# Kernel optimization log

Measured on AMD Instinct MI355X. Metric: run time of the kernel, lower is better.

The kernel has to match this reference:

```python
import jax, jax.numpy as jnp
import numpy as np

B, T, C, H = 2, 4096, 1024, 16
D = C // H
SEGMENTS = ((512, 1), (1024, 2), (2048, 4))  # (segment_length w, dilation r) per LongNet config


def setup_inputs() -> dict:
    key = jax.random.key(0)
    ks = jax.random.split(key, 12)
    s = 0.02
    return {
        "x": jax.random.normal(ks[0], (B, T, C), jnp.float32),
        # outer fused qkv projection (c_attn), stored as [in, out] so y = x @ W + b
        "c_attn_w": jax.random.normal(ks[1], (C, 3 * C), jnp.float32) * s,
        "c_attn_b": jnp.zeros((3 * C,), jnp.float32),
        # inner torchscale MultiheadAttention projections
        "q_w": jax.random.normal(ks[2], (C, C), jnp.float32) * s,
        "q_b": jnp.zeros((C,), jnp.float32),
        "k_w": jax.random.normal(ks[3], (C, C), jnp.float32) * s,
        "k_b": jnp.zeros((C,), jnp.float32),
        "v_w": jax.random.normal(ks[4], (C, C), jnp.float32) * s,
        "v_b": jnp.zeros((C,), jnp.float32),
        "o_w": jax.random.normal(ks[5], (C, C), jnp.float32) * s,
        "o_b": jnp.zeros((C,), jnp.float32),
    }


def _branch(q, k, v, w, r):
    """One dilated-attention branch: segment length w, dilation r.
    q,k,v: [B,H,T,D] (q pre-scaled). Heads use offset = head % r (LongNet).
    Returns (out_full [B,H,T,D], lse_full [B,H,T]) scattered back to full positions.
    """
    b, h_, t, d = q.shape
    n_seg, eff = t // w, w // r
    h = jnp.arange(h_)
    idx = (h % r)[:, None] + jnp.arange(eff)[None, :] * r            # [H, eff] within-segment indices
    pos = jnp.arange(n_seg)[None, :, None] * w + idx[:, None, :]     # [H, n_seg, eff] absolute positions
    hh = h[:, None, None]
    qg = q[:, hh, pos]                                               # [B,H,n_seg,eff,D]
    kg = k[:, hh, pos]
    vg = v[:, hh, pos]
    scores = jnp.einsum('bhsid,bhsjd->bhsij', qg, kg)
    causal = jnp.tril(jnp.ones((eff, eff), bool))                    # order preserved under strided subsampling
    scores = jnp.where(causal, scores, jnp.finfo(scores.dtype).min)
    m = scores.max(-1, keepdims=True)
    p = jnp.exp(scores - m)
    s = p.sum(-1, keepdims=True)
    o = jnp.einsum('bhsij,bhsjd->bhsid', p, vg) / s
    lse = m[..., 0] + jnp.log(s[..., 0])                             # [B,H,n_seg,eff]
    out_full = jnp.zeros((b, h_, t, d), q.dtype).at[:, hh, pos].set(o)
    lse_full = jnp.full((b, h_, t), -1e30, q.dtype).at[:, hh, pos].set(lse)
    return out_full, lse_full


def _forward(x, c_attn_w, c_attn_b, q_w, q_b, k_w, k_b, v_w, v_b, o_w, o_b):
    b, t, c = x.shape
    qkv = x @ c_attn_w + c_attn_b
    qx, kx, vx = jnp.split(qkv, 3, axis=-1)
    q = (qx @ q_w + q_b).reshape(b, t, H, D).transpose(0, 2, 1, 3) * (D ** -0.5)
    k = (kx @ k_w + k_b).reshape(b, t, H, D).transpose(0, 2, 1, 3)
    v = (vx @ v_w + v_b).reshape(b, t, H, D).transpose(0, 2, 1, 3)
    outs, lses = zip(*[_branch(q, k, v, w, r) for w, r in SEGMENTS])
    O = jnp.stack(outs)                                              # [S,B,H,T,D]
    L = jnp.stack(lses)                                              # [S,B,H,T]
    # LongNet combination: weight each branch by its softmax denominator (via lse)
    m = L.max(0)
    wts = jnp.exp(L - m)                                             # [S,B,H,T]
    y = (wts[..., None] * O).sum(0) / wts.sum(0)[..., None]          # [B,H,T,D]
    y = y.transpose(0, 2, 1, 3).reshape(b, t, c)
    return y @ o_w + o_b


def reference(x, c_attn_w, c_attn_b, q_w, q_b, k_w, k_b, v_w, v_b, o_w, o_b):
    return _forward(x, c_attn_w, c_attn_b, q_w, q_b, k_w, k_b, v_w, v_b, o_w, o_b)
```

## Files before the change

### kernel.cpp

```cpp
#include <hip/hip_runtime.h>
#include <hip/hip_bf16.h>

typedef __bf16 bf16x8 __attribute__((ext_vector_type(8)));
typedef float  f32x4  __attribute__((ext_vector_type(4)));

__device__ __forceinline__ unsigned short f2bf(float f) {
    union { float f; unsigned int u; } v; v.f = f;
    return (unsigned short)((v.u + 0x8000u) >> 16);
}
__device__ __forceinline__ float bf2f(unsigned short h) {
    union { unsigned int u; float f; } v; v.u = ((unsigned int)h) << 16;
    return v.f;
}

typedef __attribute__((address_space(3))) unsigned int lds_u32_t;
typedef const __attribute__((address_space(1))) unsigned int glb_u32_t;
__device__ __forceinline__ void gl_lds16(const void* g, void* l) {
    __builtin_amdgcn_global_load_lds((glb_u32_t*)g, (lds_u32_t*)l, 16, 0, 0);
}

__global__ void k_cast(const float* __restrict__ in, unsigned short* __restrict__ out, int n) {
    int i = (blockIdx.x * blockDim.x + threadIdx.x) * 4;
    if (i + 3 < n) {
        float4 v = *reinterpret_cast<const float4*>(in + i);
        ushort4 o;
        o.x = f2bf(v.x); o.y = f2bf(v.y); o.z = f2bf(v.z); o.w = f2bf(v.w);
        *reinterpret_cast<ushort4*>(out + i) = o;
    }
}

__global__ void k_transpose4(const float* __restrict__ s0, const float* __restrict__ s1,
                             const float* __restrict__ s2, const float* __restrict__ s3,
                             unsigned short* __restrict__ d0, unsigned short* __restrict__ d1,
                             unsigned short* __restrict__ d2, unsigned short* __restrict__ d3) {
    __shared__ float tile[32][33];
    int z = blockIdx.z;
    const float* in = (z == 0) ? s0 : (z == 1) ? s1 : (z == 2) ? s2 : s3;
    unsigned short* out = (z == 0) ? d0 : (z == 1) ? d1 : (z == 2) ? d2 : d3;
    int n0 = blockIdx.x * 32, k0 = blockIdx.y * 32;
    int tx = threadIdx.x, ty = threadIdx.y;
    #pragma unroll
    for (int i = 0; i < 4; ++i)
        tile[ty + i * 8][tx] = in[(size_t)(k0 + ty + i * 8) * 1024 + n0 + tx];
    __syncthreads();
    #pragma unroll
    for (int i = 0; i < 4; ++i)
        out[(size_t)(n0 + ty + i * 8) * 1024 + k0 + tx] = f2bf(tile[tx][ty + i * 8]);
}

__global__ __launch_bounds__(256) void k_gemm(
    const unsigned short* __restrict__ A, int lda,
    const unsigned short* __restrict__ Bt, int ldb,
    const float* __restrict__ bias,
    void* __restrict__ out,
    int M, int N, int K, int mode, float scale)
{
    __shared__ unsigned short As[128 * 32];
    __shared__ unsigned short Bs[128 * 32];
    int tid  = threadIdx.x;
    int lane = tid & 63, wv = tid >> 6;
    int quad = lane >> 4, l16 = lane & 15;

    int nwg = gridDim.x * gridDim.y;
    int lin = blockIdx.y * gridDim.x + blockIdx.x;
    int bx = blockIdx.x, by = blockIdx.y;
    if ((nwg & 7) == 0) {
        int swz = (lin & 7) * (nwg >> 3) + (lin >> 3);
        bx = swz % gridDim.x;
        by = swz / gridDim.x;
    }
    int bm = by * 128, bn = bx * 128;
    int wm = (wv >> 1) * 64,  wn = (wv & 1) * 64;

    f32x4 acc[4][4] = {};
    int srow = tid >> 2, scol = (tid & 3) * 8;

    for (int k0 = 0; k0 < K; k0 += 32) {
        #pragma unroll
        for (int s = 0; s < 2; ++s) {
            int row = s * 64 + srow;
            gl_lds16(&A[(size_t)(bm + row) * lda + k0 + scol], &As[(s * 256 + wv * 64) * 8]);
            gl_lds16(&Bt[(size_t)(bn + row) * ldb + k0 + scol], &Bs[(s * 256 + wv * 64) * 8]);
        }
        __syncthreads();
        bf16x8 af[4], bfv[4];
        #pragma unroll
        for (int mi = 0; mi < 4; ++mi)
            af[mi] = *reinterpret_cast<const bf16x8*>(&As[(wm + mi * 16 + l16) * 32 + quad * 8]);
        #pragma unroll
        for (int ni = 0; ni < 4; ++ni)
            bfv[ni] = *reinterpret_cast<const bf16x8*>(&Bs[(wn + ni * 16 + l16) * 32 + quad * 8]);
        #pragma unroll
        for (int mi = 0; mi < 4; ++mi)
            #pragma unroll
            for (int ni = 0; ni < 4; ++ni)
                acc[mi][ni] = __builtin_amdgcn_mfma_f32_16x16x32_bf16(bfv[ni], af[mi], acc[mi][ni], 0, 0, 0);
        __syncthreads();
    }

    #pragma unroll
    for (int mi = 0; mi < 4; ++mi) {
        int row = bm + wm + mi * 16 + l16;
        #pragma unroll
        for (int ni = 0; ni < 4; ++ni) {
            int col0 = bn + wn + ni * 16 + quad * 4;
            float4 b4 = *reinterpret_cast<const float4*>(&bias[col0]);
            float v0 = (acc[mi][ni][0] + b4.x) * scale;
            float v1 = (acc[mi][ni][1] + b4.y) * scale;
            float v2 = (acc[mi][ni][2] + b4.z) * scale;
            float v3 = (acc[mi][ni][3] + b4.w) * scale;
            if (mode == 0) {
                ushort4 o4; o4.x = f2bf(v0); o4.y = f2bf(v1); o4.z = f2bf(v2); o4.w = f2bf(v3);
                *reinterpret_cast<ushort4*>(&reinterpret_cast<unsigned short*>(out)[(size_t)row * N + col0]) = o4;
            } else {
                float4 o4; o4.x = v0; o4.y = v1; o4.z = v2; o4.w = v3;
                *reinterpret_cast<float4*>(&reinterpret_cast<float*>(out)[(size_t)row * N + col0]) = o4;
            }
        }
    }
}

__global__ __launch_bounds__(256) void k_foldw(
    const unsigned short* __restrict__ wT3,
    const unsigned short* __restrict__ WcB,
    unsigned short* __restrict__ Weff)
{
    __shared__ unsigned short As[128 * 32];
    __shared__ unsigned short Bs[128 * 32];
    int z = blockIdx.z;
    const unsigned short* A  = wT3 + (size_t)z * 1024 * 1024;
    const unsigned short* Bt = WcB + z * 1024;
    unsigned short* out = Weff + (size_t)z * 1024 * 1024;
    float scale = (z == 0) ? 0.1803368801f : 1.f;

    int tid  = threadIdx.x;
    int lane = tid & 63, wv = tid >> 6;
    int quad = lane >> 4, l16 = lane & 15;
    int bm = blockIdx.y * 128, bn = blockIdx.x * 128;
    int wm = (wv >> 1) * 64,  wn = (wv & 1) * 64;

    f32x4 acc[4][4] = {};
    int srow = tid >> 2, scol = (tid & 3) * 8;

    for (int k0 = 0; k0 < 1024; k0 += 32) {
        #pragma unroll
        for (int s = 0; s < 2; ++s) {
            int row = s * 64 + srow;
            gl_lds16(&A[(size_t)(bm + row) * 1024 + k0 + scol], &As[(s * 256 + wv * 64) * 8]);
            gl_lds16(&Bt[(size_t)(bn + row) * 3072 + k0 + scol], &Bs[(s * 256 + wv * 64) * 8]);
        }
        __syncthreads();
        bf16x8 af[4], bfv[4];
        #pragma unroll
        for (int mi = 0; mi < 4; ++mi)
            af[mi] = *reinterpret_cast<const bf16x8*>(&As[(wm + mi * 16 + l16) * 32 + quad * 8]);
        #pragma unroll
        for (int ni = 0; ni < 4; ++ni)
            bfv[ni] = *reinterpret_cast<const bf16x8*>(&Bs[(wn + ni * 16 + l16) * 32 + quad * 8]);
        #pragma unroll
        for (int mi = 0; mi < 4; ++mi)
            #pragma unroll
            for (int ni = 0; ni < 4; ++ni)
                acc[mi][ni] = __builtin_amdgcn_mfma_f32_16x16x32_bf16(bfv[ni], af[mi], acc[mi][ni], 0, 0, 0);
        __syncthreads();
    }

    #pragma unroll
    for (int mi = 0; mi < 4; ++mi) {
        int row = bm + wm + mi * 16 + l16;
        #pragma unroll
        for (int ni = 0; ni < 4; ++ni) {
            int col0 = bn + wn + ni * 16 + quad * 4;
            ushort4 o4;
            o4.x = f2bf(acc[mi][ni][0] * scale);
            o4.y = f2bf(acc[mi][ni][1] * scale);
            o4.z = f2bf(acc[mi][ni][2] * scale);
            o4.w = f2bf(acc[mi][ni][3] * scale);
            *reinterpret_cast<ushort4*>(&out[(size_t)row * 1024 + col0]) = o4;
        }
    }
}

__global__ void k_foldb(const unsigned short* __restrict__ wT3, const float* __restrict__ bc,
                        const float* __restrict__ qb, const float* __restrict__ kb,
                        const float* __restrict__ vb, float* __restrict__ beff)
{
    int id = blockIdx.x * blockDim.x + threadIdx.x;
    int z = id >> 10, n = id & 1023;
    const unsigned short* row = wT3 + (size_t)z * 1024 * 1024 + (size_t)n * 1024;
    const float* b2 = (z == 0) ? qb : (z == 1) ? kb : vb;
    float s = 0.f;
    for (int c = 0; c < 1024; ++c) s += bc[z * 1024 + c] * bf2f(row[c]);
    s += b2[n];
    if (z == 0) s *= 0.1803368801f;
    beff[id] = s;
}

__global__ __launch_bounds__(256) void k_gemm3(
    const unsigned short* __restrict__ A,
    const unsigned short* __restrict__ Weff,
    const float* __restrict__ beff,
    unsigned short* __restrict__ Qg, unsigned short* __restrict__ Kg,
    unsigned short* __restrict__ Vtg)
{
    __shared__ unsigned short As[128 * 32];
    __shared__ unsigned short Bs[128 * 32];

    int tid  = threadIdx.x;
    int lane = tid & 63, wv = tid >> 6;
    int quad = lane >> 4, l16 = lane & 15;

    int nwg = gridDim.x * gridDim.y * gridDim.z;
    int lin = (blockIdx.z * gridDim.y + blockIdx.y) * gridDim.x + blockIdx.x;
    int swz = (lin & 7) * (nwg >> 3) + (lin >> 3);
    int bx  = swz % gridDim.x;
    int tmp = swz / gridDim.x;
    int by  = tmp % gridDim.y;
    int z   = tmp / gridDim.y;

    const unsigned short* Bt = Weff + (size_t)z * 1024 * 1024;
    const float* bias = beff + z * 1024;

    int bm = by * 128, bn = bx * 128;
    int wm = (wv >> 1) * 64,  wn = (wv & 1) * 64;

    f32x4 acc[4][4] = {};
    int srow = tid >> 2, scol = (tid & 3) * 8;

    for (int k0 = 0; k0 < 1024; k0 += 32) {
        #pragma unroll
        for (int s = 0; s < 2; ++s) {
            int row = s * 64 + srow;
            gl_lds16(&A[(size_t)(bm + row) * 1024 + k0 + scol], &As[(s * 256 + wv * 64) * 8]);
            gl_lds16(&Bt[(size_t)(bn + row) * 1024 + k0 + scol], &Bs[(s * 256 + wv * 64) * 8]);
        }
        __syncthreads();
        bf16x8 af[4], bfv[4];
        #pragma unroll
        for (int mi = 0; mi < 4; ++mi)
            af[mi] = *reinterpret_cast<const bf16x8*>(&As[(wm + mi * 16 + l16) * 32 + quad * 8]);
        #pragma unroll
        for (int ni = 0; ni < 4; ++ni)
            bfv[ni] = *reinterpret_cast<const bf16x8*>(&Bs[(wn + ni * 16 + l16) * 32 + quad * 8]);
        if (z < 2) {
            #pragma unroll
            for (int mi = 0; mi < 4; ++mi)
                #pragma unroll
                for (int ni = 0; ni < 4; ++ni)
                    acc[mi][ni] = __builtin_amdgcn_mfma_f32_16x16x32_bf16(bfv[ni], af[mi], acc[mi][ni], 0, 0, 0);
        } else {
            #pragma unroll
            for (int mi = 0; mi < 4; ++mi)
                #pragma unroll
                for (int ni = 0; ni < 4; ++ni)
                    acc[mi][ni] = __builtin_amdgcn_mfma_f32_16x16x32_bf16(af[mi], bfv[ni], acc[mi][ni], 0, 0, 0);
        }
        __syncthreads();
    }

    if (z < 2) {
        unsigned short* dst = (z == 0) ? Qg : Kg;
        int hh = (bn + wn) >> 6;
        #pragma unroll
        for (int mi = 0; mi < 4; ++mi) {
            int trow = bm + wm + mi * 16 + l16;
            int b = trow >> 12, t = trow & 4095;
            int bh = b * 16 + hh;
            int slot0 = t >> 9,         idx0 = t & 511;
            int slot1 = 8 + (t >> 10),  idx1 = (t & 1023) >> 1;
            int slot2 = 12 + (t >> 11), idx2 = (t & 2047) >> 2;
            bool c1 = ((t ^ hh) & 1) == 0;
            bool c2 = ((t ^ hh) & 3) == 0;
            size_t r0 = ((size_t)(slot0 * 32 + bh) * 512 + idx0) * 64;
            size_t r1 = ((size_t)(slot1 * 32 + bh) * 512 + idx1) * 64;
            size_t r2 = ((size_t)(slot2 * 32 + bh) * 512 + idx2) * 64;
            #pragma unroll
            for (int ni = 0; ni < 4; ++ni) {
                int d0 = ni * 16 + quad * 4;
                float4 b4 = *reinterpret_cast<const float4*>(&bias[bn + wn + d0]);
                ushort4 o4;
                o4.x = f2bf(acc[mi][ni][0] + b4.x);
                o4.y = f2bf(acc[mi][ni][1] + b4.y);
                o4.z = f2bf(acc[mi][ni][2] + b4.z);
                o4.w = f2bf(acc[mi][ni][3] + b4.w);
                *reinterpret_cast<ushort4*>(&dst[r0 + d0]) = o4;
                if (c1) *reinterpret_cast<ushort4*>(&dst[r1 + d0]) = o4;
                if (c2) *reinterpret_cast<ushort4*>(&dst[r2 + d0]) = o4;
            }
        }
    } else {
        int h_glob = (bn + wn) >> 6;
        int j1 = h_glob & 1;
        int j2 = h_glob & 3;
        #pragma unroll
        for (int ni = 0; ni < 4; ++ni) {
            int d = ni * 16 + l16;
            float bsv = bias[bn + wn + d];
            #pragma unroll
            for (int mi = 0; mi < 4; ++mi) {
                int t0g = bm + wm + mi * 16 + quad * 4;
                int b = t0g >> 12, t0 = t0g & 4095;
                int bh = b * 16 + h_glob;
                unsigned short val[4];
                #pragma unroll
                for (int ri = 0; ri < 4; ++ri) val[ri] = f2bf(acc[mi][ni][ri] + bsv);
                {
                    int slot = t0 >> 9;
                    size_t base = ((size_t)(slot * 32 + bh) * 64 + d) * 512 + (t0 & 511);
                    *reinterpret_cast<ushort4*>(&Vtg[base]) = *reinterpret_cast<const ushort4*>(val);
                }
                {
                    int slot = 8 + (t0 >> 10);
                    int idx = ((t0 + j1) & 1023) >> 1;
                    size_t base = ((size_t)(slot * 32 + bh) * 64 + d) * 512 + idx;
                    ushort2 o2; o2.x = val[j1]; o2.y = val[j1 + 2];
                    *reinterpret_cast<ushort2*>(&Vtg[base]) = o2;
                }
                {
                    int slot = 12 + (t0 >> 11);
                    int idx = ((t0 + j2) & 2047) >> 2;
                    Vtg[((size_t)(slot * 32 + bh) * 64 + d) * 512 + idx] = val[j2];
                }
            }
        }
    }
}

__global__ __launch_bounds__(256, 3) void k_attn(
    const unsigned short* __restrict__ Qg,
    const unsigned short* __restrict__ Kg,
    const unsigned short* __restrict__ Vtg,
    unsigned short* __restrict__ Og,
    float* __restrict__ Lg)
{
    __shared__ unsigned short Ks[2][64 * 72];
    __shared__ unsigned short Vs[2][64 * 72];

    int tid  = threadIdx.x;
    int lane = tid & 63, wv = tid >> 6;
    int quad = lane >> 4, l16 = lane & 15;
    int q8   = quad << 3;
    int pq = blockIdx.x, ys = blockIdx.y, bh = blockIdx.z;
    int jt_end = 2 * (3 - pq) + 1;
    size_t sb = (size_t)(ys * 32 + bh) * (512 * 64);
    const unsigned short* qp = Qg + sb;
    const unsigned short* kp = Kg + sb;
    const unsigned short* vp = Vtg + sb;
    unsigned short* op = Og + sb;
    float* lp = Lg + (size_t)(ys * 32 + bh) * 512;

    int rw[2] = { pq * 128 + wv * 32, (3 - pq) * 128 + wv * 32 };

    int srow = tid >> 3, sc8 = (tid & 7) * 8;
    int prow = ((srow >> 2) & 1) * 16 + ((srow >> 3) & 3) * 4 + (srow & 3);
    uint4 kr[2], vr[2];
    {
        #pragma unroll
        for (int s = 0; s < 2; ++s) {
            int row = s * 32 + srow;
            kr[s] = *reinterpret_cast<const uint4*>(&kp[(size_t)row * 64 + sc8]);
            vr[s] = *reinterpret_cast<const uint4*>(&vp[(size_t)row * 512 + sc8]);
        }
    }

    bf16x8 qf[2][2][2];
    #pragma unroll
    for (int qi = 0; qi < 2; ++qi)
        #pragma unroll
        for (int m16 = 0; m16 < 2; ++m16)
            #pragma unroll
            for (int kk = 0; kk < 2; ++kk)
                qf[qi][m16][kk] = *reinterpret_cast<const bf16x8*>(
                    &qp[(size_t)(rw[qi] + m16 * 16 + l16) * 64 + kk * 32 + quad * 8]);

    f32x4 acc[2][2][4] = {};
    float l4[2][2] = {};

    for (int jt = 0; jt <= jt_end; ++jt) {
        unsigned short* Kb = &Ks[jt & 1][0];
        unsigned short* Vb = &Vs[jt & 1][0];
        #pragma unroll
        for (int s = 0; s < 2; ++s) {
            *reinterpret_cast<uint4*>(&Kb[(s * 32 + prow) * 72 + sc8]) = kr[s];
            *reinterpret_cast<uint4*>(&Vb[(s * 32 + srow) * 72 + sc8]) = vr[s];
        }
        if (jt < jt_end) {
            #pragma unroll
            for (int s = 0; s < 2; ++s) {
                int row = s * 32 + srow;
                kr[s] = *reinterpret_cast<const uint4*>(&kp[(size_t)((jt + 1) * 64 + row) * 64 + sc8]);
                vr[s] = *reinterpret_cast<const uint4*>(&vp[(size_t)row * 512 + (jt + 1) * 64 + sc8]);
            }
        }
        __syncthreads();

        #pragma unroll
        for (int qi = 0; qi < 2; ++qi) {
            #pragma unroll
            for (int m16 = 0; m16 < 2; ++m16) {
                int rowbase = rw[qi] + m16 * 16;
                if (jt * 64 > rowbase + 15) continue;

                f32x4 sacc[4];
                __builtin_amdgcn_s_setprio(1);
                #pragma unroll
                for (int nt = 0; nt < 4; ++nt) {
                    bf16x8 b0 = *reinterpret_cast<const bf16x8*>(&Kb[(nt * 16 + l16) * 72 + quad * 8]);
                    bf16x8 b1 = *reinterpret_cast<const bf16x8*>(&Kb[(nt * 16 + l16) * 72 + 32 + quad * 8]);
                    f32x4 s4 = {};
                    s4 = __builtin_amdgcn_mfma_f32_16x16x32_bf16(b0, qf[qi][m16][0], s4, 0, 0, 0);
                    s4 = __builtin_amdgcn_mfma_f32_16x16x32_bf16(b1, qf[qi][m16][1], s4, 0, 0, 0);
                    sacc[nt] = s4;
                }
                __builtin_amdgcn_s_setprio(0);

                if (jt * 64 + 63 > rowbase) {
                    int qrow = rowbase + l16;
                    #pragma unroll
                    for (int nt = 0; nt < 4; ++nt)
                        #pragma unroll
                        for (int ri = 0; ri < 4; ++ri) {
                            int kj = jt * 64 + (nt >> 1) * 32 + (nt & 1) * 4 + q8 + ri;
                            if (kj > qrow) sacc[nt][ri] = -1e30f;
                        }
                }
                float ls = 0.f;
                #pragma unroll
                for (int nt = 0; nt < 4; ++nt)
                    #pragma unroll
                    for (int ri = 0; ri < 4; ++ri) {
                        float p = __builtin_amdgcn_exp2f(sacc[nt][ri]);
                        sacc[nt][ri] = p;
                        ls += p;
                    }
                l4[qi][m16] += ls;

                union { unsigned int u[4]; bf16x8 v; } p0u, p1u;
                asm("v_cvt_pk_bf16_f32 %0, %1, %2" : "=v"(p0u.u[0]) : "v"(sacc[0][0]), "v"(sacc[0][1]));
                asm("v_cvt_pk_bf16_f32 %0, %1, %2" : "=v"(p0u.u[1]) : "v"(sacc[0][2]), "v"(sacc[0][3]));
                asm("v_cvt_pk_bf16_f32 %0, %1, %2" : "=v"(p0u.u[2]) : "v"(sacc[1][0]), "v"(sacc[1][1]));
                asm("v_cvt_pk_bf16_f32 %0, %1, %2" : "=v"(p0u.u[3]) : "v"(sacc[1][2]), "v"(sacc[1][3]));
                asm("v_cvt_pk_bf16_f32 %0, %1, %2" : "=v"(p1u.u[0]) : "v"(sacc[2][0]), "v"(sacc[2][1]));
                asm("v_cvt_pk_bf16_f32 %0, %1, %2" : "=v"(p1u.u[1]) : "v"(sacc[2][2]), "v"(sacc[2][3]));
                asm("v_cvt_pk_bf16_f32 %0, %1, %2" : "=v"(p1u.u[2]) : "v"(sacc[3][0]), "v"(sacc[3][1]));
                asm("v_cvt_pk_bf16_f32 %0, %1, %2" : "=v"(p1u.u[3]) : "v"(sacc[3][2]), "v"(sacc[3][3]));

                __builtin_amdgcn_s_setprio(1);
                #pragma unroll
                for (int dt = 0; dt < 4; ++dt) {
                    bf16x8 v0 = *reinterpret_cast<const bf16x8*>(&Vb[(dt * 16 + l16) * 72 + quad * 8]);
                    bf16x8 v1 = *reinterpret_cast<const bf16x8*>(&Vb[(dt * 16 + l16) * 72 + 32 + quad * 8]);
                    f32x4 a4 = acc[qi][m16][dt];
                    a4 = __builtin_amdgcn_mfma_f32_16x16x32_bf16(p0u.v, v0, a4, 0, 0, 0);
                    a4 = __builtin_amdgcn_mfma_f32_16x16x32_bf16(p1u.v, v1, a4, 0, 0, 0);
                    acc[qi][m16][dt] = a4;
                }
                __builtin_amdgcn_s_setprio(0);
            }
        }
    }

    #pragma unroll
    for (int qi = 0; qi < 2; ++qi)
        #pragma unroll
        for (int m16 = 0; m16 < 2; ++m16) {
            int rowb = rw[qi] + m16 * 16;
            float L = l4[qi][m16];
            L += __shfl_xor(L, 16);
            L += __shfl_xor(L, 32);
            float inv[4];
            #pragma unroll
            for (int ri = 0; ri < 4; ++ri)
                inv[ri] = 1.f / __shfl(L, quad * 4 + ri);
            #pragma unroll
            for (int dt = 0; dt < 4; ++dt)
                #pragma unroll
                for (int ri = 0; ri < 4; ++ri) {
                    int row = rowb + quad * 4 + ri;
                    op[(size_t)row * 64 + dt * 16 + l16] = f2bf(acc[qi][m16][dt][ri] * inv[ri]);
                }
            if (lane < 16)
                lp[rowb + l16] = __logf(L);
        }
}

__global__ void k_combine(const unsigned short* __restrict__ Og,
                          const float* __restrict__ Lg,
                          unsigned short* __restrict__ yb)
{
    int g   = blockIdx.x * blockDim.x + threadIdx.x;
    int row = g >> 3;
    int d0  = (g & 7) * 8;
    int bh = row >> 12, t = row & 4095;
    int b = bh >> 4, h = bh & 15;

    int slot0 = t >> 9,         idx0 = t & 511;
    int slot1 = 8 + (t >> 10),  idx1 = (t & 1023) >> 1;
    int slot2 = 12 + (t >> 11), idx2 = (t & 2047) >> 2;
    size_t r0 = (size_t)(slot0 * 32 + bh) * 512 + idx0;
    size_t r1 = (size_t)(slot1 * 32 + bh) * 512 + idx1;
    size_t r2 = (size_t)(slot2 * 32 + bh) * 512 + idx2;
    bool c1 = ((t ^ h) & 1) == 0;
    bool c2 = ((t ^ h) & 3) == 0;

    float L0 = Lg[r0];
    float L1 = c1 ? Lg[r1] : -1e30f;
    float L2 = c2 ? Lg[r2] : -1e30f;
    float m  = fmaxf(L0, fmaxf(L1, L2));
    float w0 = __expf(L0 - m), w1 = __expf(L1 - m), w2 = __expf(L2 - m);
    float inv = 1.f / (w0 + w1 + w2);

    uint4 v0 = *reinterpret_cast<const uint4*>(&Og[r0 * 64 + d0]);
    uint4 v1 = *reinterpret_cast<const uint4*>(&Og[r1 * 64 + d0]);
    uint4 v2 = *reinterpret_cast<const uint4*>(&Og[r2 * 64 + d0]);
    const unsigned short* p0 = reinterpret_cast<const unsigned short*>(&v0);
    const unsigned short* p1 = reinterpret_cast<const unsigned short*>(&v1);
    const unsigned short* p2 = reinterpret_cast<const unsigned short*>(&v2);
    unsigned short o[8];
    #pragma unroll
    for (int u = 0; u < 8; ++u)
        o[u] = f2bf((w0 * bf2f(p0[u]) + w1 * bf2f(p1[u]) + w2 * bf2f(p2[u])) * inv);
    size_t yidx = (((size_t)b * 4096 + t) * 1024) + (size_t)h * 64 + d0;
    *reinterpret_cast<uint4*>(&yb[yidx]) = *reinterpret_cast<const uint4*>(o);
}

extern "C" void kernel_launch(void* const* d_in, const int* in_sizes, int n_in,
                              void* d_out, int out_size, void* d_ws, size_t ws_size,
                              hipStream_t stream)
{
    const float* x        = (const float*)d_in[0];
    const float* c_attn_w = (const float*)d_in[1];
    const float* c_attn_b = (const float*)d_in[2];
    const float* q_w      = (const float*)d_in[3];
    const float* q_b      = (const float*)d_in[4];
    const float* k_w      = (const float*)d_in[5];
    const float* k_b      = (const float*)d_in[6];
    const float* v_w      = (const float*)d_in[7];
    const float* v_b      = (const float*)d_in[8];
    const float* o_w      = (const float*)d_in[9];
    const float* o_b      = (const float*)d_in[10];

    char* ws = (char*)d_ws;
    size_t off = 0;
    auto alloc = [&](size_t bytes) -> char* {
        char* p = ws + off; off += (bytes + 255) & ~(size_t)255; return p;
    };
    const size_t GSZ = 14ull * 32 * 512 * 64;
    unsigned short* xb    = (unsigned short*)alloc(8192ull * 1024 * 2);
    unsigned short* WcB   = (unsigned short*)alloc(1024ull * 3072 * 2);
    unsigned short* wqT   = (unsigned short*)alloc(1024ull * 1024 * 2);
    unsigned short* wkT   = (unsigned short*)alloc(1024ull * 1024 * 2);
    unsigned short* wvT   = (unsigned short*)alloc(1024ull * 1024 * 2);
    unsigned short* woT   = (unsigned short*)alloc(1024ull * 1024 * 2);
    unsigned short* Weff  = (unsigned short*)alloc(3ull * 1024 * 1024 * 2);
    float*          beff  = (float*)alloc(3ull * 1024 * 4);
    unsigned short* Qg    = (unsigned short*)alloc(GSZ * 2);
    unsigned short* Kg    = (unsigned short*)alloc(GSZ * 2);
    unsigned short* Vtg   = (unsigned short*)alloc(GSZ * 2);
    unsigned short* Og    = (unsigned short*)alloc(GSZ * 2);
    float*          Lg    = (float*)alloc(14ull * 32 * 512 * 4);
    unsigned short* yb    = xb;
    (void)wkT; (void)wvT;

    k_cast<<<(8192 * 1024) / 1024, 256, 0, stream>>>(x, xb, 8192 * 1024);
    k_cast<<<(1024 * 3072) / 1024, 256, 0, stream>>>(c_attn_w, WcB, 1024 * 3072);
    k_transpose4<<<dim3(32, 32, 4), dim3(32, 8), 0, stream>>>(q_w, k_w, v_w, o_w, wqT, wkT, wvT, woT);
    k_foldw<<<dim3(8, 8, 3), 256, 0, stream>>>(wqT, WcB, Weff);
    k_foldb<<<12, 256, 0, stream>>>(wqT, c_attn_b, q_b, k_b, v_b, beff);
    k_gemm3<<<dim3(8, 64, 3), 256, 0, stream>>>(xb, Weff, beff, Qg, Kg, Vtg);
    k_attn<<<dim3(2, 14, 32), 256, 0, stream>>>(Qg, Kg, Vtg, Og, Lg);
    k_combine<<<4096, 256, 0, stream>>>(Og, Lg, yb);
    k_gemm<<<dim3(8, 64), 256, 0, stream>>>(yb, 1024, woT, 1024, o_b, d_out, 8192, 1024, 1024, 2, 1.f);
}
```

Baseline: 382.0 us.

## Stage QKV epilogue through LDS for coalesced scatter; parallelize bias fold per wave

The QKV GEMM epilogue now writes the bf16 tile into padded shared memory and then emits 16-byte coalesced stores for each dilated-segment layout (Q/K rows and transposed V), replacing scattered 8/4/2-byte strided global writes. Separately, the bias-folding kernel goes from one thread per output with a serial 1024-long loop to one wave per output with vectorized loads and a shuffle reduction, launched across 768 blocks. The cost is a larger LDS footprint, an extra barrier, and strided LDS gathers for the dilated V layouts.

```diff
diff --git a/kernel.cpp b/kernel.cpp
--- a/kernel.cpp
+++ b/kernel.cpp
@@ -181,19 +181,35 @@
     }
 }
 
-__global__ void k_foldb(const unsigned short* __restrict__ wT3, const float* __restrict__ bc,
-                        const float* __restrict__ qb, const float* __restrict__ kb,
-                        const float* __restrict__ vb, float* __restrict__ beff)
+__global__ __launch_bounds__(256) void k_foldb(
+    const unsigned short* __restrict__ wT3, const float* __restrict__ bc,
+    const float* __restrict__ qb, const float* __restrict__ kb,
+    const float* __restrict__ vb, float* __restrict__ beff)
 {
-    int id = blockIdx.x * blockDim.x + threadIdx.x;
+    int wv = threadIdx.x >> 6, lane = threadIdx.x & 63;
+    int id = blockIdx.x * 4 + wv;
     int z = id >> 10, n = id & 1023;
     const unsigned short* row = wT3 + (size_t)z * 1024 * 1024 + (size_t)n * 1024;
-    const float* b2 = (z == 0) ? qb : (z == 1) ? kb : vb;
+    const float* bcz = bc + z * 1024;
     float s = 0.f;
-    for (int c = 0; c < 1024; ++c) s += bc[z * 1024 + c] * bf2f(row[c]);
-    s += b2[n];
-    if (z == 0) s *= 0.1803368801f;
-    beff[id] = s;
+    #pragma unroll
+    for (int it = 0; it < 2; ++it) {
+        int c0 = it * 512 + lane * 8;
+        uint4 v = *reinterpret_cast<const uint4*>(&row[c0]);
+        const unsigned short* pv = reinterpret_cast<const unsigned short*>(&v);
+        float4 f0 = *reinterpret_cast<const float4*>(&bcz[c0]);
+        float4 f1 = *reinterpret_cast<const float4*>(&bcz[c0 + 4]);
+        s += f0.x * bf2f(pv[0]) + f0.y * bf2f(pv[1]) + f0.z * bf2f(pv[2]) + f0.w * bf2f(pv[3]);
+        s += f1.x * bf2f(pv[4]) + f1.y * bf2f(pv[5]) + f1.z * bf2f(pv[6]) + f1.w * bf2f(pv[7]);
+    }
+    s += __shfl_xor(s, 1); s += __shfl_xor(s, 2); s += __shfl_xor(s, 4);
+    s += __shfl_xor(s, 8); s += __shfl_xor(s, 16); s += __shfl_xor(s, 32);
+    if (lane == 0) {
+        const float* b2 = (z == 0) ? qb : (z == 1) ? kb : vb;
+        float r = s + b2[n];
+        if (z == 0) r *= 0.1803368801f;
+        beff[id] = r;
+    }
 }
 
 __global__ __launch_bounds__(256) void k_gemm3(
@@ -203,8 +219,10 @@
     unsigned short* __restrict__ Qg, unsigned short* __restrict__ Kg,
     unsigned short* __restrict__ Vtg)
 {
-    __shared__ unsigned short As[128 * 32];
-    __shared__ unsigned short Bs[128 * 32];
+    __shared__ unsigned short smem[16896];
+    unsigned short* As = smem;
+    unsigned short* Bs = smem + 4096;
+    const int TS = 132;
 
     int tid  = threadIdx.x;
     int lane = tid & 63, wv = tid >> 6;
@@ -213,10 +231,10 @@
     int nwg = gridDim.x * gridDim.y * gridDim.z;
     int lin = (blockIdx.z * gridDim.y + blockIdx.y) * gridDim.x + blockIdx.x;
     int swz = (lin & 7) * (nwg >> 3) + (lin >> 3);
-    int bx  = swz % gridDim.x;
-    int tmp = swz / gridDim.x;
-    int by  = tmp % gridDim.y;
-    int z   = tmp / gridDim.y;
+    int bx  = swz & 7;
+    int tmp = swz >> 3;
+    int by  = tmp & 63;
+    int z   = tmp >> 6;
 
     const unsigned short* Bt = Weff + (size_t)z * 1024 * 1024;
     const float* bias = beff + z * 1024;
@@ -258,70 +276,121 @@
         __syncthreads();
     }
 
+    unsigned short* T = smem;
+    int b  = bm >> 12, t0 = bm & 4095;
+    int h0 = bn >> 6;
+    int slot0 = t0 >> 9;
+    int slot1 = 8 + (t0 >> 10);
+    int slot2 = 12 + (t0 >> 11);
+
     if (z < 2) {
         unsigned short* dst = (z == 0) ? Qg : Kg;
-        int hh = (bn + wn) >> 6;
         #pragma unroll
         for (int mi = 0; mi < 4; ++mi) {
-            int trow = bm + wm + mi * 16 + l16;
-            int b = trow >> 12, t = trow & 4095;
-            int bh = b * 16 + hh;
-            int slot0 = t >> 9,         idx0 = t & 511;
-            int slot1 = 8 + (t >> 10),  idx1 = (t & 1023) >> 1;
-            int slot2 = 12 + (t >> 11), idx2 = (t & 2047) >> 2;
-            bool c1 = ((t ^ hh) & 1) == 0;
-            bool c2 = ((t ^ hh) & 3) == 0;
-            size_t r0 = ((size_t)(slot0 * 32 + bh) * 512 + idx0) * 64;
-            size_t r1 = ((size_t)(slot1 * 32 + bh) * 512 + idx1) * 64;
-            size_t r2 = ((size_t)(slot2 * 32 + bh) * 512 + idx2) * 64;
+            int tl = wm + mi * 16 + l16;
             #pragma unroll
             for (int ni = 0; ni < 4; ++ni) {
-                int d0 = ni * 16 + quad * 4;
-                float4 b4 = *reinterpret_cast<const float4*>(&bias[bn + wn + d0]);
+                int dl0 = wn + ni * 16 + quad * 4;
+                float4 b4 = *reinterpret_cast<const float4*>(&bias[bn + dl0]);
                 ushort4 o4;
                 o4.x = f2bf(acc[mi][ni][0] + b4.x);
                 o4.y = f2bf(acc[mi][ni][1] + b4.y);
                 o4.z = f2bf(acc[mi][ni][2] + b4.z);
                 o4.w = f2bf(acc[mi][ni][3] + b4.w);
-                *reinterpret_cast<ushort4*>(&dst[r0 + d0]) = o4;
-                if (c1) *reinterpret_cast<ushort4*>(&dst[r1 + d0]) = o4;
-                if (c2) *reinterpret_cast<ushort4*>(&dst[r2 + d0]) = o4;
+                *reinterpret_cast<ushort4*>(&T[tl * TS + dl0]) = o4;
             }
         }
+        __syncthreads();
+        #pragma unroll
+        for (int rep = 0; rep < 8; ++rep) {
+            int c = rep * 256 + tid;
+            int h = c >> 10, rr = c & 1023;
+            int tl = rr >> 3, dseg = (rr & 7) * 8;
+            int bh = b * 16 + h0 + h;
+            size_t base = ((size_t)(slot0 * 32 + bh) * 512 + (t0 & 511) + tl) * 64;
+            *reinterpret_cast<uint4*>(&dst[base + dseg]) =
+                *reinterpret_cast<const uint4*>(&T[tl * TS + h * 64 + dseg]);
+        }
+        #pragma unroll
+        for (int rep = 0; rep < 4; ++rep) {
+            int c = rep * 256 + tid;
+            int h = c >> 9, rr = c & 511;
+            int i = rr >> 3, dseg = (rr & 7) * 8;
+            int hh = h0 + h;
+            int bh = b * 16 + hh;
+            int tl = 2 * i + (hh & 1);
+            size_t base = ((size_t)(slot1 * 32 + bh) * 512 + ((t0 & 1023) >> 1) + i) * 64;
+            *reinterpret_cast<uint4*>(&dst[base + dseg]) =
+                *reinterpret_cast<const uint4*>(&T[tl * TS + h * 64 + dseg]);
+        }
+        #pragma unroll
+        for (int rep = 0; rep < 2; ++rep) {
+            int c = rep * 256 + tid;
+            int h = c >> 8, rr = c & 255;
+            int i = rr >> 3, dseg = (rr & 7) * 8;
+            int hh = h0 + h;
+            int bh = b * 16 + hh;
+            int tl = 4 * i + (hh & 3);
+            size_t base = ((size_t)(slot2 * 32 + bh) * 512 + ((t0 & 2047) >> 2) + i) * 64;
+            *reinterpret_cast<uint4*>(&dst[base + dseg]) =
+                *reinterpret_cast<const uint4*>(&T[tl * TS + h * 64 + dseg]);
+        }
     } else {
-        int h_glob = (bn + wn) >> 6;
-        int j1 = h_glob & 1;
-        int j2 = h_glob & 3;
         #pragma unroll
         for (int ni = 0; ni < 4; ++ni) {
-            int d = ni * 16 + l16;
-            float bsv = bias[bn + wn + d];
+            int dl = wn + ni * 16 + l16;
+            float bsv = bias[bn + dl];
             #pragma unroll
             for (int mi = 0; mi < 4; ++mi) {
-                int t0g = bm + wm + mi * 16 + quad * 4;
-                int b = t0g >> 12, t0 = t0g & 4095;
-                int bh = b * 16 + h_glob;
-                unsigned short val[4];
-                #pragma unroll
-                for (int ri = 0; ri < 4; ++ri) val[ri] = f2bf(acc[mi][ni][ri] + bsv);
-                {
-                    int slot = t0 >> 9;
-                    size_t base = ((size_t)(slot * 32 + bh) * 64 + d) * 512 + (t0 & 511);
-                    *reinterpret_cast<ushort4*>(&Vtg[base]) = *reinterpret_cast<const ushort4*>(val);
-                }
-                {
-                    int slot = 8 + (t0 >> 10);
-                    int idx = ((t0 + j1) & 1023) >> 1;
-                    size_t base = ((size_t)(slot * 32 + bh) * 64 + d) * 512 + idx;
-                    ushort2 o2; o2.x = val[j1]; o2.y = val[j1 + 2];
-                    *reinterpret_cast<ushort2*>(&Vtg[base]) = o2;
-                }
-                {
-                    int slot = 12 + (t0 >> 11);
-                    int idx = ((t0 + j2) & 2047) >> 2;
-                    Vtg[((size_t)(slot * 32 + bh) * 64 + d) * 512 + idx] = val[j2];
-                }
+                int tl0 = wm + mi * 16 + quad * 4;
+                ushort4 o4;
+                o4.x = f2bf(acc[mi][ni][0] + bsv);
+                o4.y = f2bf(acc[mi][ni][1] + bsv);
+                o4.z = f2bf(acc[mi][ni][2] + bsv);
+                o4.w = f2bf(acc[mi][ni][3] + bsv);
+                *reinterpret_cast<ushort4*>(&T[dl * TS + tl0]) = o4;
             }
+        }
+        __syncthreads();
+        #pragma unroll
+        for (int rep = 0; rep < 8; ++rep) {
+            int c = rep * 256 + tid;
+            int h = c >> 10, rr = c & 1023;
+            int d = rr >> 4, seg = (rr & 15) * 8;
+            int bh = b * 16 + h0 + h;
+            size_t base = ((size_t)(slot0 * 32 + bh) * 64 + d) * 512 + (t0 & 511);
+            *reinterpret_cast<uint4*>(&Vtg[base + seg]) =
+                *reinterpret_cast<const uint4*>(&T[(h * 64 + d) * TS + seg]);
+        }
+        #pragma unroll
+        for (int rep = 0; rep < 4; ++rep) {
+            int c = rep * 256 + tid;
+            int h = c >> 9, rr = c & 511;
+            int d = rr >> 3, seg = rr & 7;
+            int hh = h0 + h;
+            int bh = b * 16 + hh;
+            int p = hh & 1;
+            const unsigned short* srow = &T[(h * 64 + d) * TS];
+            unsigned short buf[8];
+            #pragma unroll
+            for (int j = 0; j < 8; ++j) buf[j] = srow[p + 2 * (seg * 8 + j)];
+            size_t base = ((size_t)(slot1 * 32 + bh) * 64 + d) * 512 + ((t0 & 1023) >> 1);
+            *reinterpret_cast<uint4*>(&Vtg[base + seg * 8]) = *reinterpret_cast<const uint4*>(buf);
+        }
+        #pragma unroll
+        for (int rep = 0; rep < 2; ++rep) {
+            int c = rep * 256 + tid;
+            int h = c >> 8, rr = c & 255;
+            int d = rr >> 2, seg = rr & 3;
+            int hh = h0 + h;
+            int bh = b * 16 + hh;
+            int p = hh & 3;
+            const unsigned short* srow = &T[(h * 64 + d) * TS];
+            unsigned short buf[8];
+            #pragma unroll
+            for (int j = 0; j < 8; ++j) buf[j] = srow[p + 4 * (seg * 8 + j)];
+            size_t base = ((size_t)(slot2 * 32 + bh) * 64 + d) * 512 + ((t0 & 2047) >> 2);
+            *reinterpret_cast<uint4*>(&Vtg[base + seg * 8]) = *reinterpret_cast<const uint4*>(buf);
         }
     }
 }
@@ -566,7 +635,7 @@
     k_cast<<<(1024 * 3072) / 1024, 256, 0, stream>>>(c_attn_w, WcB, 1024 * 3072);
     k_transpose4<<<dim3(32, 32, 4), dim3(32, 8), 0, stream>>>(q_w, k_w, v_w, o_w, wqT, wkT, wvT, woT);
     k_foldw<<<dim3(8, 8, 3), 256, 0, stream>>>(wqT, WcB, Weff);
-    k_foldb<<<12, 256, 0, stream>>>(wqT, c_attn_b, q_b, k_b, v_b, beff);
+    k_foldb<<<768, 256, 0, stream>>>(wqT, c_attn_b, q_b, k_b, v_b, beff);
     k_gemm3<<<dim3(8, 64, 3), 256, 0, stream>>>(xb, Weff, beff, Qg, Kg, Vtg);
     k_attn<<<dim3(2, 14, 32), 256, 0, stream>>>(Qg, Kg, Vtg, Og, Lg);
     k_combine<<<4096, 256, 0, stream>>>(Og, Lg, yb);
```

New measurement: 327.6 us. -14.2%, faster.
